# Performance work log

Hardware: AMD Instinct MI355X
Metric: run time of the kernel (lower is better)

## Reference

```python
import jax, jax.numpy as jnp
import numpy as np

B, C, H, W = 4, 128, 128, 128
HEADS, DHEAD = 8, C // 8
N = H * W
NEG_SLOPE = 0.2
LN_EPS = 1e-5


def _build_grid_edges(h, w):
    # 3x3 neighborhood including self (matches the torch double loop),
    # then append N extra self loops (add_self_loops in the module).
    rows, cols = [], []
    for r in range(h):
        for c in range(w):
            idx = r * w + c
            for dr in (-1, 0, 1):
                for dc in (-1, 0, 1):
                    nr, nc = r + dr, c + dc
                    if 0 <= nr < h and 0 <= nc < w:
                        rows.append(idx)
                        cols.append(nr * w + nc)
    rows += list(range(h * w))
    cols += list(range(h * w))
    return np.asarray(rows, np.int32), np.asarray(cols, np.int32)

_SRC_NP, _DST_NP = _build_grid_edges(H, W)  # PyG: messages flow src -> dst
SRC = jnp.asarray(_SRC_NP)
DST = jnp.asarray(_DST_NP)


def setup_inputs() -> dict:
    key = jax.random.key(0)
    ks = jax.random.split(key, 7)
    s_lin = 1.0 / np.sqrt(C)
    return {
        "x": jax.random.normal(ks[0], (B, C, H, W), jnp.float32),
        "W_lin": jax.random.normal(ks[1], (C, HEADS * DHEAD), jnp.float32) * s_lin,
        "att_src": jax.random.normal(ks[2], (HEADS, DHEAD), jnp.float32) * s_lin,
        "att_dst": jax.random.normal(ks[3], (HEADS, DHEAD), jnp.float32) * s_lin,
        "bias": jnp.zeros((C,), jnp.float32),
        "gamma": jnp.ones((C,), jnp.float32),
        "beta": jnp.zeros((C,), jnp.float32),
    }


def _gat_forward(x, W_lin, att_src, att_dst, bias, gamma, beta):
    b = x.shape[0]
    x_nodes = x.reshape(b, C, N).transpose(0, 2, 1)            # [B,N,C]
    xp = (x_nodes @ W_lin).reshape(b, N, HEADS, DHEAD)          # [B,N,H,D]
    a_src = jnp.einsum('bnhd,hd->bnh', xp, att_src)             # [B,N,H]
    a_dst = jnp.einsum('bnhd,hd->bnh', xp, att_dst)
    score = jax.nn.leaky_relu(a_src[:, SRC] + a_dst[:, DST], NEG_SLOPE)  # [B,E,H]

    def seg_softmax(s):  # [E,H] softmax over edges grouped by DST
        m = jax.ops.segment_max(s, DST, num_segments=N)
        e = jnp.exp(s - m[DST])
        den = jax.ops.segment_sum(e, DST, num_segments=N)
        return e / den[DST]

    alpha = jax.vmap(seg_softmax)(score)                        # [B,E,H]
    msg = xp[:, SRC] * alpha[..., None]                         # [B,E,H,D]
    agg = jax.vmap(lambda m: jax.ops.segment_sum(m, DST, num_segments=N))(msg)
    out = agg.reshape(b, N, C) + bias                           # GATConv bias
    out = jax.nn.elu(out)
    # LayerNorm over channel dim
    mu = out.mean(-1, keepdims=True)
    var = out.var(-1, keepdims=True)
    out = (out - mu) * jax.lax.rsqrt(var + LN_EPS) * gamma + beta
    return out.transpose(0, 2, 1).reshape(b, C, H, W)


def reference(x, W_lin, att_src, att_dst, bias, gamma, beta):
    return _gat_forward(x, W_lin, att_src, att_dst, bias, gamma, beta)
```

## Files before the change

### kernel.cpp

```cpp
#include <hip/hip_runtime.h>
#include <hip/hip_fp16.h>
#include <stdint.h>

#define BATCH  4
#define CCH    128
#define GRID_H 128
#define GRID_W 128
#define NNODE  (GRID_H*GRID_W)
#define NHEAD  8
#define DH     16
#define WPAD   68
#define WROWS  144

typedef __attribute__((ext_vector_type(8))) short short8;
typedef __attribute__((ext_vector_type(4))) float f32x4;
typedef __attribute__((ext_vector_type(4))) unsigned u32x4;

__device__ inline unsigned packbf(float a, float b){
    unsigned r;
    asm("v_cvt_pk_bf16_f32 %0, %1, %2" : "=v"(r) : "v"(a), "v"(b));
    return r;
}
__device__ inline unsigned packhf(float a, float b){
    unsigned r;
    asm("v_cvt_pkrtz_f16_f32 %0, %1, %2" : "=v"(r) : "v"(a), "v"(b));
    return r;
}

__global__ void kW(const float* __restrict__ Wl, const float* __restrict__ attS,
                   const float* __restrict__ attD, unsigned* __restrict__ Wb)
{
    __shared__ float Wa[8][16];
    const int t = threadIdx.x;
    const int cbase = blockIdx.x * 8;
    if (t < 128){
        int cl = t >> 4, j = t & 15;
        const float* av = (j < 8 ? attS + j*DH : attD + (j-8)*DH);
        const float* wr = Wl + (size_t)(cbase + cl)*CCH + (j & 7)*DH;
        float s = 0.f;
        #pragma unroll
        for (int d = 0; d < DH; ++d) s += wr[d]*av[d];
        Wa[cl][j] = s;
    }
    __syncthreads();
    for (int it = 0; it < 3; ++it){
        int flat = it*256 + t;
        if (flat < 576){
            int k2l = flat / 144, co = flat % 144;
            int k2 = blockIdx.x*4 + k2l;
            float w0, w1;
            if (co < CCH){
                w0 = Wl[(size_t)(2*k2)*CCH + co];
                w1 = Wl[(size_t)(2*k2+1)*CCH + co];
            } else {
                w0 = Wa[2*k2l][co-CCH];
                w1 = Wa[2*k2l+1][co-CCH];
            }
            Wb[co*WPAD + k2] = packbf(w0, w1);
        }
    }
}

__global__ __launch_bounds__(256, 3) void kA(
    const float* __restrict__ x, const unsigned* __restrict__ Wbg,
    __half* __restrict__ xpb, float* __restrict__ scS, float* __restrict__ scD)
{
    __shared__ __align__(16) unsigned WbL[WROWS*WPAD];

    const int t  = threadIdx.x;
    const int b  = blockIdx.y;
    const int bx = blockIdx.x;
    const int row = (bx & 7)*16 + (bx >> 3);
    const int n0  = row * GRID_W;

    #pragma unroll
    for (int it = 0; it < 10; ++it){
        int f4 = it*256 + t;
        if (f4 < (WROWS*WPAD)/4)
            *(u32x4*)(&WbL[f4*4]) = *(const u32x4*)(Wbg + (size_t)f4*4);
    }
    __syncthreads();

    const int w = t >> 6, lane = t & 63;
    const int col = lane & 15, q = lane >> 4;
    const float* xb = x + (size_t)b*CCH*NNODE;
    const int nA = n0 + (2*w+0)*16 + col;
    const int nB = n0 + (2*w+1)*16 + col;

    f32x4 acc[2][9];
    #pragma unroll
    for (int mi = 0; mi < 2; ++mi)
        #pragma unroll
        for (int ct = 0; ct < 9; ++ct) acc[mi][ct] = (f32x4)(0.f);

    float xrA[8], xrB[8], x2A[8], x2B[8];
    #pragma unroll
    for (int j = 0; j < 8; ++j){
        const size_t co = (size_t)(q*8 + j)*NNODE;
        xrA[j] = __builtin_nontemporal_load(&xb[co + nA]);
        xrB[j] = __builtin_nontemporal_load(&xb[co + nB]);
    }

    union U { u32x4 u; short8 s; };
    #pragma unroll
    for (int kc = 0; kc < 4; ++kc){
        if (kc < 3){
            #pragma unroll
            for (int j = 0; j < 8; ++j){
                const size_t co = (size_t)((kc+1)*32 + q*8 + j)*NNODE;
                x2A[j] = __builtin_nontemporal_load(&xb[co + nA]);
                x2B[j] = __builtin_nontemporal_load(&xb[co + nB]);
            }
        }
        U fa0, fa1;
        #pragma unroll
        for (int i = 0; i < 4; ++i){
            fa0.u[i] = packbf(xrA[2*i], xrA[2*i+1]);
            fa1.u[i] = packbf(xrB[2*i], xrB[2*i+1]);
        }
        const int kof = kc*16 + q*4;
        #pragma unroll
        for (int ct = 0; ct < 9; ++ct){
            U fb; fb.u = *(const u32x4*)(&WbL[(ct*16+col)*WPAD + kof]);
            acc[0][ct] = __builtin_amdgcn_mfma_f32_16x16x32_bf16(fa0.s, fb.s, acc[0][ct], 0, 0, 0);
            acc[1][ct] = __builtin_amdgcn_mfma_f32_16x16x32_bf16(fa1.s, fb.s, acc[1][ct], 0, 0, 0);
        }
        #pragma unroll
        for (int j = 0; j < 8; ++j){ xrA[j] = x2A[j]; xrB[j] = x2B[j]; }
    }

    __half* xr = xpb + (size_t)b*NNODE*CCH;
    float*  sS = scS + (size_t)b*NNODE*NHEAD;
    float*  sD = scD + (size_t)b*NNODE*NHEAD;
    #pragma unroll
    for (int mi = 0; mi < 2; ++mi){
        #pragma unroll
        for (int r = 0; r < 4; ++r){
            const int n = n0 + (2*w+mi)*16 + q*4 + r;
            #pragma unroll
            for (int ct = 0; ct < 8; ++ct)
                xr[(size_t)n*CCH + ct*16 + col] = __float2half(acc[mi][ct][r]);
            const float v = acc[mi][8][r];
            if (col < 8) sS[(size_t)n*NHEAD + col]     = v;
            else         sD[(size_t)n*NHEAD + col - 8] = v;
        }
    }
}

__device__ inline void kb_issue(int n, const float* __restrict__ scSb,
                                const float* __restrict__ scDb,
                                const uint2* __restrict__ xvb, int h, int l2,
                                int* vm, float aS[9], float* aD, uint2 xv[9])
{
    const int rr = n >> 7, cc = n & 127;
    const bool vU = rr > 0, vD = rr < GRID_H-1, vL = cc > 0, vR = cc < GRID_W-1;
    int m = 0;
    #pragma unroll
    for (int e = 0; e < 9; ++e){
        const int dr = e/3 - 1, dc = e%3 - 1;
        const bool vr_ = (dr < 0) ? vU : (dr > 0 ? vD : true);
        const bool vc_ = (dc < 0) ? vL : (dc > 0 ? vR : true);
        const bool v = vr_ && vc_;
        const int src = v ? (n + dr*GRID_W + dc) : n;
        m |= ((int)v) << e;
        aS[e] = scSb[src*NHEAD + h];
        xv[e] = xvb[(size_t)src*32 + l2];
    }
    *aD = scDb[n*NHEAD + h];
    *vm = m;
}

__global__ __launch_bounds__(256, 4) void kB(
    const __half* __restrict__ xpb, const float* __restrict__ scS,
    const float* __restrict__ scD,
    const float* __restrict__ bias, const float* __restrict__ gamma,
    const float* __restrict__ beta, float* __restrict__ out)
{
    __shared__ float outT[CCH][65];
    const int t = threadIdx.x, w = t >> 6, lane = t & 63;
    const int h2 = lane >> 5, l2 = lane & 31;
    const int b  = blockIdx.y;
    const int bx = blockIdx.x;
    const int xcd = bx & 7, mid = (bx >> 3) & 7, cq = bx >> 6;
    const int r0 = (xcd*8 + mid)*2, c0 = cq*32;
    const int n0 = r0*GRID_W + c0;

    const uint2* xvb  = (const uint2*)(xpb + (size_t)b*NNODE*CCH);
    const float* scSb = scS + (size_t)b*NNODE*NHEAD;
    const float* scDb = scD + (size_t)b*NNODE*NHEAD;
    const int h = l2 >> 2;
    const f32x4 bi = *(const f32x4*)(bias  + 4*l2);
    const f32x4 ga = *(const f32x4*)(gamma + 4*l2);
    const f32x4 be = *(const f32x4*)(beta  + 4*l2);

    float aSP[2][9]; uint2 xvP[2][9]; float aDP[2]; int vmP[2];

    #define NODE(i) ({ const int nl_ = w*16 + 2*(i) + h2; \
                       n0 + (nl_ >> 5)*GRID_W + (nl_ & 31); })

    kb_issue(NODE(0), scSb, scDb, xvb, h, l2, &vmP[0], aSP[0], &aDP[0], xvP[0]);

    #pragma unroll
    for (int ii = 0; ii < 4; ++ii){
        #pragma unroll
        for (int ph = 0; ph < 2; ++ph){
            const int i = 2*ii + ph;
            const int cur = i & 1;
            if (i + 1 < 8)
                kb_issue(NODE(i+1), scSb, scDb, xvb, h, l2,
                         &vmP[cur^1], aSP[cur^1], &aDP[cur^1], xvP[cur^1]);

            const int vm = vmP[cur];
            const float* aS = aSP[cur];
            const uint2*  xv = xvP[cur];
            const float ad = aDP[cur];
            const int nl = w*16 + 2*i + h2;

            float s[9], mx = -1e30f;
            #pragma unroll
            for (int e = 0; e < 9; ++e){
                float sv = aS[e] + ad;
                sv = fmaxf(sv, 0.2f*sv);
                s[e] = ((vm >> e) & 1) ? sv : -1e30f;
                mx = fmaxf(mx, s[e]);
            }
            float wt[9], den = 0.f;
            #pragma unroll
            for (int e = 0; e < 9; ++e){
                float ex = __expf(s[e] - mx);
                ex = ((vm >> e) & 1) ? ex : 0.f;
                wt[e] = ex; den += ex;
            }
            den += wt[4];
            const float inv = __builtin_amdgcn_rcpf(den);

            union HU { unsigned u; __half2 h; };
            HU a01, a23; a01.u = 0u; a23.u = 0u;
            #pragma unroll
            for (int e = 0; e < 9; ++e){
                float f = wt[e] * inv;
                if (e == 4) f += f;
                HU hf; hf.u = packhf(f, f);
                HU lo; lo.u = xv[e].x;
                HU hi; hi.u = xv[e].y;
                a01.h = __hfma2(hf.h, lo.h, a01.h);
                a23.h = __hfma2(hf.h, hi.h, a23.h);
            }
            const float a0 = __low2float(a01.h), a1 = __high2float(a01.h);
            const float a2 = __low2float(a23.h), a3 = __high2float(a23.h);

            float o0 = a0 + bi[0], o1 = a1 + bi[1], o2 = a2 + bi[2], o3 = a3 + bi[3];
            o0 = o0 > 0.f ? o0 : __expf(o0) - 1.f;
            o1 = o1 > 0.f ? o1 : __expf(o1) - 1.f;
            o2 = o2 > 0.f ? o2 : __expf(o2) - 1.f;
            o3 = o3 > 0.f ? o3 : __expf(o3) - 1.f;

            float sm = (o0 + o1) + (o2 + o3);
            float sq = o0*o0 + o1*o1 + o2*o2 + o3*o3;
            #pragma unroll
            for (int off = 1; off <= 16; off <<= 1){
                sm += __shfl_xor(sm, off, 64);
                sq += __shfl_xor(sq, off, 64);
            }
            const float mu  = sm * (1.f/128.f);
            float var = sq * (1.f/128.f) - mu*mu;
            var = var < 0.f ? 0.f : var;
            const float rstd = __builtin_amdgcn_rsqf(var + 1e-5f);
            outT[4*l2+0][nl] = (o0 - mu)*rstd*ga[0] + be[0];
            outT[4*l2+1][nl] = (o1 - mu)*rstd*ga[1] + be[1];
            outT[4*l2+2][nl] = (o2 - mu)*rstd*ga[2] + be[2];
            outT[4*l2+3][nl] = (o3 - mu)*rstd*ga[3] + be[3];
        }
    }
    #undef NODE
    __syncthreads();

    float* ob = out + (size_t)b*CCH*NNODE + n0;
    const int poff = (lane >> 5)*GRID_W + (lane & 31);
    #pragma unroll
    for (int it = 0; it < 32; ++it){
        int c = it*4 + w;
        __builtin_nontemporal_store(outT[c][lane], &ob[(size_t)c*NNODE + poff]);
    }
}

extern "C" void kernel_launch(void* const* d_in, const int* in_sizes, int n_in,
                              void* d_out, int out_size, void* d_ws, size_t ws_size,
                              hipStream_t stream)
{
    const float* x    = (const float*)d_in[0];
    const float* Wl   = (const float*)d_in[1];
    const float* attS = (const float*)d_in[2];
    const float* attD = (const float*)d_in[3];
    const float* bias = (const float*)d_in[4];
    const float* gamma= (const float*)d_in[5];
    const float* beta = (const float*)d_in[6];
    float* out = (float*)d_out;

    __half* xpb = (__half*)d_ws;
    float*  scS = (float*)((char*)d_ws + (size_t)BATCH*NNODE*CCH*2);
    float*  scD = scS + (size_t)BATCH*NNODE*NHEAD;
    unsigned* Wb = (unsigned*)(scD + (size_t)BATCH*NNODE*NHEAD);

    kW<<<dim3(16),               256, 0, stream>>>(Wl, attS, attD, Wb);
    kA<<<dim3(NNODE/128, BATCH), 256, 0, stream>>>(x, Wb, xpb, scS, scD);
    kB<<<dim3(NNODE/64,  BATCH), 256, 0, stream>>>(xpb, scS, scD, bias, gamma, beta, out);
}
```

Measured before the change: 119.6 us.

## Stage halo tile of projected features and scores in LDS for neighbor gather

The aggregation kernel now cooperatively loads a 4x34-node halo tile of fp16 projected features and source scores, plus the destination scores, into shared memory. The 3x3 neighbor gather then reads from LDS instead of issuing nine global loads per node through a register double-buffered prefetch. This removes redundant global and L2 traffic, since each node is otherwise fetched by up to nine neighbors. In exchange it uses about 40KB of extra LDS and adds a barrier before compute, and launch bounds drop to 2 blocks per CU, which lowers occupancy and removes the load/compute overlap.

Result: slower. 127.8 us (+6.8%).

```diff
diff --git a/kernel.cpp b/kernel.cpp
--- a/kernel.cpp
+++ b/kernel.cpp
@@ -26,6 +26,7 @@
     asm("v_cvt_pkrtz_f16_f32 %0, %1, %2" : "=v"(r) : "v"(a), "v"(b));
     return r;
 }
+__device__ inline int clamp127(int v){ return v < 0 ? 0 : (v > 127 ? 127 : v); }
 
 __global__ void kW(const float* __restrict__ Wl, const float* __restrict__ attS,
                    const float* __restrict__ attD, unsigned* __restrict__ Wb)
@@ -147,132 +148,139 @@
     }
 }
 
-__device__ inline void kb_issue(int n, const float* __restrict__ scSb,
-                                const float* __restrict__ scDb,
-                                const uint2* __restrict__ xvb, int h, int l2,
-                                int* vm, float aS[9], float* aD, uint2 xv[9])
-{
-    const int rr = n >> 7, cc = n & 127;
-    const bool vU = rr > 0, vD = rr < GRID_H-1, vL = cc > 0, vR = cc < GRID_W-1;
-    int m = 0;
-    #pragma unroll
-    for (int e = 0; e < 9; ++e){
-        const int dr = e/3 - 1, dc = e%3 - 1;
-        const bool vr_ = (dr < 0) ? vU : (dr > 0 ? vD : true);
-        const bool vc_ = (dc < 0) ? vL : (dc > 0 ? vR : true);
-        const bool v = vr_ && vc_;
-        const int src = v ? (n + dr*GRID_W + dc) : n;
-        m |= ((int)v) << e;
-        aS[e] = scSb[src*NHEAD + h];
-        xv[e] = xvb[(size_t)src*32 + l2];
-    }
-    *aD = scDb[n*NHEAD + h];
-    *vm = m;
-}
-
-__global__ __launch_bounds__(256, 4) void kB(
+__global__ __launch_bounds__(256, 2) void kB(
     const __half* __restrict__ xpb, const float* __restrict__ scS,
     const float* __restrict__ scD,
     const float* __restrict__ bias, const float* __restrict__ gamma,
     const float* __restrict__ beta, float* __restrict__ out)
 {
+    __shared__ __align__(16) __half xpH[4*34*CCH];
+    __shared__ __align__(16) float  scSH[4*34*NHEAD];
+    __shared__ __align__(16) float  scDH[64*NHEAD];
     __shared__ float outT[CCH][65];
+
     const int t = threadIdx.x, w = t >> 6, lane = t & 63;
-    const int h2 = lane >> 5, l2 = lane & 31;
+    const int hw = t >> 5, l2 = t & 31;
     const int b  = blockIdx.y;
     const int bx = blockIdx.x;
     const int xcd = bx & 7, mid = (bx >> 3) & 7, cq = bx >> 6;
     const int r0 = (xcd*8 + mid)*2, c0 = cq*32;
     const int n0 = r0*GRID_W + c0;
 
-    const uint2* xvb  = (const uint2*)(xpb + (size_t)b*NNODE*CCH);
-    const float* scSb = scS + (size_t)b*NNODE*NHEAD;
-    const float* scDb = scD + (size_t)b*NNODE*NHEAD;
+    const __half* xb   = xpb + (size_t)b*NNODE*CCH;
+    const float*  scSb = scS + (size_t)b*NNODE*NHEAD;
+    const float*  scDb = scD + (size_t)b*NNODE*NHEAD;
+
+    #pragma unroll
+    for (int hr = 0; hr < 4; ++hr){
+        const int sr = clamp127(r0 - 1 + hr);
+        #pragma unroll
+        for (int k = 0; k < 3; ++k){
+            const int flat = k*256 + t;
+            if (flat < 544){
+                const int node = flat >> 4, chunk = flat & 15;
+                const int sc = clamp127(c0 - 1 + node);
+                u32x4 v = *(const u32x4*)(xb + ((size_t)(sr*GRID_W + sc))*CCH + chunk*8);
+                *(u32x4*)((char*)xpH + ((size_t)(hr*34 + node)*256 + chunk*16)) = v;
+            }
+        }
+    }
+    if (t < 136){
+        const int hr = t / 34, hc = t % 34;
+        const int sr = clamp127(r0 - 1 + hr);
+        const int sc = clamp127(c0 - 1 + hc);
+        const float* sp = scSb + (size_t)(sr*GRID_W + sc)*NHEAD;
+        *(f32x4*)&scSH[t*8]     = *(const f32x4*)sp;
+        *(f32x4*)&scSH[t*8 + 4] = *(const f32x4*)(sp + 4);
+    }
+    if (t < 64){
+        const int tr = t >> 5, tc = t & 31;
+        const float* sp = scDb + (size_t)((r0+tr)*GRID_W + c0+tc)*NHEAD;
+        *(f32x4*)&scDH[t*8]     = *(const f32x4*)sp;
+        *(f32x4*)&scDH[t*8 + 4] = *(const f32x4*)(sp + 4);
+    }
+    __syncthreads();
+
     const int h = l2 >> 2;
     const f32x4 bi = *(const f32x4*)(bias  + 4*l2);
     const f32x4 ga = *(const f32x4*)(gamma + 4*l2);
     const f32x4 be = *(const f32x4*)(beta  + 4*l2);
 
-    float aSP[2][9]; uint2 xvP[2][9]; float aDP[2]; int vmP[2];
-
-    #define NODE(i) ({ const int nl_ = w*16 + 2*(i) + h2; \
-                       n0 + (nl_ >> 5)*GRID_W + (nl_ & 31); })
-
-    kb_issue(NODE(0), scSb, scDb, xvb, h, l2, &vmP[0], aSP[0], &aDP[0], xvP[0]);
-
-    #pragma unroll
-    for (int ii = 0; ii < 4; ++ii){
-        #pragma unroll
-        for (int ph = 0; ph < 2; ++ph){
-            const int i = 2*ii + ph;
-            const int cur = i & 1;
-            if (i + 1 < 8)
-                kb_issue(NODE(i+1), scSb, scDb, xvb, h, l2,
-                         &vmP[cur^1], aSP[cur^1], &aDP[cur^1], xvP[cur^1]);
-
-            const int vm = vmP[cur];
-            const float* aS = aSP[cur];
-            const uint2*  xv = xvP[cur];
-            const float ad = aDP[cur];
-            const int nl = w*16 + 2*i + h2;
-
-            float s[9], mx = -1e30f;
-            #pragma unroll
-            for (int e = 0; e < 9; ++e){
-                float sv = aS[e] + ad;
-                sv = fmaxf(sv, 0.2f*sv);
-                s[e] = ((vm >> e) & 1) ? sv : -1e30f;
-                mx = fmaxf(mx, s[e]);
-            }
-            float wt[9], den = 0.f;
-            #pragma unroll
-            for (int e = 0; e < 9; ++e){
-                float ex = __expf(s[e] - mx);
-                ex = ((vm >> e) & 1) ? ex : 0.f;
-                wt[e] = ex; den += ex;
-            }
-            den += wt[4];
-            const float inv = __builtin_amdgcn_rcpf(den);
-
-            union HU { unsigned u; __half2 h; };
-            HU a01, a23; a01.u = 0u; a23.u = 0u;
-            #pragma unroll
-            for (int e = 0; e < 9; ++e){
-                float f = wt[e] * inv;
-                if (e == 4) f += f;
-                HU hf; hf.u = packhf(f, f);
-                HU lo; lo.u = xv[e].x;
-                HU hi; hi.u = xv[e].y;
-                a01.h = __hfma2(hf.h, lo.h, a01.h);
-                a23.h = __hfma2(hf.h, hi.h, a23.h);
-            }
-            const float a0 = __low2float(a01.h), a1 = __high2float(a01.h);
-            const float a2 = __low2float(a23.h), a3 = __high2float(a23.h);
-
-            float o0 = a0 + bi[0], o1 = a1 + bi[1], o2 = a2 + bi[2], o3 = a3 + bi[3];
-            o0 = o0 > 0.f ? o0 : __expf(o0) - 1.f;
-            o1 = o1 > 0.f ? o1 : __expf(o1) - 1.f;
-            o2 = o2 > 0.f ? o2 : __expf(o2) - 1.f;
-            o3 = o3 > 0.f ? o3 : __expf(o3) - 1.f;
-
-            float sm = (o0 + o1) + (o2 + o3);
-            float sq = o0*o0 + o1*o1 + o2*o2 + o3*o3;
-            #pragma unroll
-            for (int off = 1; off <= 16; off <<= 1){
-                sm += __shfl_xor(sm, off, 64);
-                sq += __shfl_xor(sq, off, 64);
-            }
-            const float mu  = sm * (1.f/128.f);
-            float var = sq * (1.f/128.f) - mu*mu;
-            var = var < 0.f ? 0.f : var;
-            const float rstd = __builtin_amdgcn_rsqf(var + 1e-5f);
-            outT[4*l2+0][nl] = (o0 - mu)*rstd*ga[0] + be[0];
-            outT[4*l2+1][nl] = (o1 - mu)*rstd*ga[1] + be[1];
-            outT[4*l2+2][nl] = (o2 - mu)*rstd*ga[2] + be[2];
-            outT[4*l2+3][nl] = (o3 - mu)*rstd*ga[3] + be[3];
-        }
-    }
-    #undef NODE
+    #pragma unroll
+    for (int i = 0; i < 8; ++i){
+        const int ln = i*8 + hw;
+        const int tr = ln >> 5, tc = ln & 31;
+        const int rg = r0 + tr, cg = c0 + tc;
+        const bool vU = rg > 0, vD = rg < GRID_H-1, vL = cg > 0, vR = cg < GRID_W-1;
+
+        const float ad = scDH[ln*8 + h];
+        uint2 xv[9]; float aS[9]; int vm = 0;
+        #pragma unroll
+        for (int e = 0; e < 9; ++e){
+            const int dr = e/3 - 1, dc = e%3 - 1;
+            const bool v = ((dr < 0) ? vU : (dr > 0 ? vD : true)) &&
+                           ((dc < 0) ? vL : (dc > 0 ? vR : true));
+            vm |= ((int)v) << e;
+            const int hnode = (tr+1+dr)*34 + (tc+1+dc);
+            xv[e] = *(const uint2*)((const char*)xpH + (size_t)hnode*256 + l2*8);
+            aS[e] = scSH[hnode*8 + h];
+        }
+
+        float s[9], mx = -1e30f;
+        #pragma unroll
+        for (int e = 0; e < 9; ++e){
+            float sv = aS[e] + ad;
+            sv = fmaxf(sv, 0.2f*sv);
+            s[e] = ((vm >> e) & 1) ? sv : -1e30f;
+            mx = fmaxf(mx, s[e]);
+        }
+        float wt[9], den = 0.f;
+        #pragma unroll
+        for (int e = 0; e < 9; ++e){
+            float ex = __expf(s[e] - mx);
+            ex = ((vm >> e) & 1) ? ex : 0.f;
+            wt[e] = ex; den += ex;
+        }
+        den += wt[4];
+        const float inv = __builtin_amdgcn_rcpf(den);
+
+        union HU { unsigned u; __half2 h; };
+        HU a01, a23; a01.u = 0u; a23.u = 0u;
+        #pragma unroll
+        for (int e = 0; e < 9; ++e){
+            float f = wt[e] * inv;
+            if (e == 4) f += f;
+            HU hf; hf.u = packhf(f, f);
+            HU lo; lo.u = xv[e].x;
+            HU hi; hi.u = xv[e].y;
+            a01.h = __hfma2(hf.h, lo.h, a01.h);
+            a23.h = __hfma2(hf.h, hi.h, a23.h);
+        }
+        const float a0 = __low2float(a01.h), a1 = __high2float(a01.h);
+        const float a2 = __low2float(a23.h), a3 = __high2float(a23.h);
+
+        float o0 = a0 + bi[0], o1 = a1 + bi[1], o2 = a2 + bi[2], o3 = a3 + bi[3];
+        o0 = o0 > 0.f ? o0 : __expf(o0) - 1.f;
+        o1 = o1 > 0.f ? o1 : __expf(o1) - 1.f;
+        o2 = o2 > 0.f ? o2 : __expf(o2) - 1.f;
+        o3 = o3 > 0.f ? o3 : __expf(o3) - 1.f;
+
+        float sm = (o0 + o1) + (o2 + o3);
+        float sq = o0*o0 + o1*o1 + o2*o2 + o3*o3;
+        #pragma unroll
+        for (int off = 1; off <= 16; off <<= 1){
+            sm += __shfl_xor(sm, off, 64);
+            sq += __shfl_xor(sq, off, 64);
+        }
+        const float mu  = sm * (1.f/128.f);
+        float var = sq * (1.f/128.f) - mu*mu;
+        var = var < 0.f ? 0.f : var;
+        const float rstd = __builtin_amdgcn_rsqf(var + 1e-5f);
+        outT[4*l2+0][ln] = (o0 - mu)*rstd*ga[0] + be[0];
+        outT[4*l2+1][ln] = (o1 - mu)*rstd*ga[1] + be[1];
+        outT[4*l2+2][ln] = (o2 - mu)*rstd*ga[2] + be[2];
+        outT[4*l2+3][ln] = (o3 - mu)*rstd*ga[3] + be[3];
+    }
     __syncthreads();
 
     float* ob = out + (size_t)b*CCH*NNODE + n0;
```
